# Kernel tuning notes

Hardware: AMD Instinct MI355X
Metric: run time of the kernel (lower is better)

The kernel has to match this reference:

```python
import jax, jax.numpy as jnp
import numpy as np

CAPACITY = 1024


def setup_inputs() -> dict:
    T, H, I, E, K = 2048, 1024, 1408, 8, 2
    key = jax.random.key(0)
    k0, k1, k2, k3, k4 = jax.random.split(key, 5)
    hidden_states = jax.random.normal(k0, (T, H), dtype=jnp.float32)
    w1 = jax.random.normal(k1, (E, 2 * I, H), dtype=jnp.float32) * 0.02  # [gate; up]
    w2 = jax.random.normal(k2, (E, H, I), dtype=jnp.float32) * 0.02
    topk_weights = jax.random.uniform(k3, (T, K), dtype=jnp.float32)
    topk_ids = jax.random.randint(k4, (T, K), 0, E, dtype=jnp.int32)
    return {"hidden_states": hidden_states, "w1": w1, "w2": w2,
            "topk_weights": topk_weights, "topk_ids": topk_ids}


def reference(hidden_states, w1, w2, topk_weights, topk_ids):
    # MoE: prepare(dispatch) -> grouped expert GEMM (silu-gated MLP) -> finalize(combine)
    T, H = hidden_states.shape
    E = w1.shape[0]
    I = w2.shape[2]
    K = topk_ids.shape[1]
    C = CAPACITY

    # ---- prepare: dispatch token copies to per-expert buffers ----
    flat_ids = topk_ids.reshape(-1)                       # (T*K,)
    onehot = jax.nn.one_hot(flat_ids, E, dtype=jnp.int32)  # (T*K, E)
    cs = jnp.cumsum(onehot, axis=0)                        # running per-expert counts
    pos = jnp.take_along_axis(cs, flat_ids[:, None], axis=1)[:, 0] - 1  # slot in expert buffer
    keep = pos < C
    pos_c = jnp.where(keep, pos, 0)

    x_flat = jnp.repeat(hidden_states, K, axis=0)          # (T*K, H)
    x_e = jnp.zeros((E, C, H), dtype=hidden_states.dtype)
    x_e = x_e.at[flat_ids, pos_c].add(jnp.where(keep[:, None], x_flat, 0.0))

    # ---- grouped expert GEMM: silu(gate) * up, then down-proj ----
    h = jnp.einsum('ech,eoh->eco', x_e, w1)                # (E, C, 2I)
    gate, up = h[..., :I], h[..., I:]
    act = jax.nn.silu(gate) * up                           # (E, C, I)
    y = jnp.einsum('eci,ehi->ech', act, w2)                # (E, C, H)

    # ---- finalize: gather back, apply router weights, reduce over top-k ----
    y_flat = y[flat_ids, pos_c] * (keep[:, None].astype(y.dtype)) \
             * topk_weights.reshape(-1, 1)                 # (T*K, H)
    out = y_flat.reshape(T, K, H).sum(axis=1)              # (T, H)
    return out.astype(hidden_states.dtype)
```

## Files before the change

kernel.cpp:

```cpp
#include <hip/hip_runtime.h>

#define NE 8
#define CAP 1024
#define HD 1024
#define ID 1408
#define TT 2048

typedef __attribute__((ext_vector_type(8))) short bf16x8;
typedef __attribute__((ext_vector_type(4))) float f32x4;
typedef unsigned short u16;
typedef unsigned int u32;
typedef unsigned long long u64;

__device__ __forceinline__ u16 f2bf(float f) {
  u32 u = __float_as_uint(f);
  u = (u + 0x7fffu + ((u >> 16) & 1u)) >> 16;
  return (u16)u;
}

__device__ __forceinline__ bf16x8 pack8(float4 a, float4 b) {
  bf16x8 r;
  r[0] = (short)f2bf(a.x); r[1] = (short)f2bf(a.y);
  r[2] = (short)f2bf(a.z); r[3] = (short)f2bf(a.w);
  r[4] = (short)f2bf(b.x); r[5] = (short)f2bf(b.y);
  r[6] = (short)f2bf(b.z); r[7] = (short)f2bf(b.w);
  return r;
}

__device__ __forceinline__ void async_cp16(const void* g, void* l) {
  __builtin_amdgcn_global_load_lds(
      (const __attribute__((address_space(1))) u32*)g,
      (__attribute__((address_space(3))) u32*)l, 16, 0, 0);
}

#define W1ROWS (NE * 2 * ID)
#define XBLK (TT * HD / 4 / 256)
__global__ __launch_bounds__(256) void prep_kernel(
    const float4* __restrict__ w1, ushort4* __restrict__ bw1,
    const float4* __restrict__ x, ushort4* __restrict__ bx,
    const int* __restrict__ ids, int* __restrict__ rowmap,
    int* __restrict__ counts) {
  int b = blockIdx.x;
  int tid = threadIdx.x;
  if (b == 0) {
    __shared__ unsigned char ids_s[TT * 2];
    __shared__ int sc[256][NE + 1];
    for (int i = tid; i < TT * 2; i += 256) ids_s[i] = (unsigned char)ids[i];
    __syncthreads();
    int base = tid * 16;
    u64 own64 = 0;
#pragma unroll
    for (int j = 0; j < 16; ++j) own64 += 1ull << (ids_s[base + j] * 8);
    int own[NE];
#pragma unroll
    for (int e = 0; e < NE; ++e) {
      own[e] = (int)((own64 >> (e * 8)) & 0xff);
      sc[tid][e] = own[e];
    }
    __syncthreads();
    for (int off = 1; off < 256; off <<= 1) {
      int v[NE];
      if (tid >= off) {
#pragma unroll
        for (int e = 0; e < NE; ++e) v[e] = sc[tid - off][e];
      }
      __syncthreads();
      if (tid >= off) {
#pragma unroll
        for (int e = 0; e < NE; ++e) sc[tid][e] += v[e];
      }
      __syncthreads();
    }
    if (tid == 255) {
#pragma unroll
      for (int e = 0; e < NE; ++e) counts[e] = sc[255][e] < CAP ? sc[255][e] : CAP;
    }
    int excl[NE];
#pragma unroll
    for (int e = 0; e < NE; ++e) excl[e] = sc[tid][e] - own[e];
    __syncthreads();
#pragma unroll
    for (int e = 0; e < NE; ++e) sc[tid][e] = excl[e];
#pragma unroll
    for (int j = 0; j < 16; ++j) {
      int f = base + j;
      int e = ids_s[f];
      int p = sc[tid][e]++;
      if (p < CAP) rowmap[e * CAP + p] = f;
    }
    return;
  }
  int bb = b - 1;
  if (bb < W1ROWS) {
    int n = bb % (2 * ID);
    int e = bb / (2 * ID);
    int j = (n < ID) ? n : (n - ID);
    int np = (j >> 4) * 32 + (j & 15) + ((n < ID) ? 0 : 16);
    float4 v = w1[((size_t)e * 2 * ID + n) * (HD / 4) + tid];
    ushort4 o;
    o.x = f2bf(v.x); o.y = f2bf(v.y); o.z = f2bf(v.z); o.w = f2bf(v.w);
    bw1[((size_t)e * 2 * ID + np) * (HD / 4) + tid] = o;
  } else {
    size_t i = (size_t)(bb - W1ROWS) * 256 + tid;
    float4 v = x[i];
    ushort4 o;
    o.x = f2bf(v.x); o.y = f2bf(v.y); o.z = f2bf(v.z); o.w = f2bf(v.w);
    bx[i] = o;
  }
}

#define G1BUF 24576
__global__ __launch_bounds__(256) void gemm1_kernel(
    const u16* __restrict__ A, const u16* __restrict__ B, u16* __restrict__ Hb,
    const int* __restrict__ rowmap, const int* __restrict__ counts,
    const float4* __restrict__ W2, bf16x8* __restrict__ bw2,
    float4* __restrict__ outz) {
  int bid = blockIdx.x;
  int tid = threadIdx.x;
  if (bid < 704) {
#pragma unroll
    for (int k2 = 0; k2 < 4; ++k2) {
      size_t base4 = ((size_t)bid * 4 + k2) * 1024;
      float4 v0 = W2[base4 + tid * 2];
      float4 v1 = W2[base4 + tid * 2 + 1];
      float4 v2 = W2[base4 + 512 + tid * 2];
      float4 v3 = W2[base4 + 512 + tid * 2 + 1];
      bf16x8* dst = bw2 + base4 / 2;
      dst[tid] = pack8(v0, v1);
      dst[256 + tid] = pack8(v2, v3);
    }
    return;
  }
  if (bid < 768) {
    size_t base = (size_t)(bid - 704) * 8192;
    float4 z = {0.f, 0.f, 0.f, 0.f};
#pragma unroll
    for (int i2 = 0; i2 < 32; ++i2) outz[base + i2 * 256 + tid] = z;
    return;
  }
  int g = bid - 768;
  int e = g & 7;
  int m0 = ((g >> 3) & 15) * 64;
  int n0 = (g >> 7) * 128;
  int count = counts[e];
  if (m0 >= count) return;
  int lane = tid & 63, wid = tid >> 6;
  int wm = wid >> 1, wn = wid & 1;
  int q = lane >> 4, lm = lane & 15;

  __shared__ __align__(16) char sm[3 * G1BUF];

  int rloc = tid >> 3;
  int chs = ((tid & 7) ^ (rloc & 7)) * 8;
  const u16* aP[2];
  const u16* bP[4];
#pragma unroll
  for (int i = 0; i < 2; ++i) {
    int gr = m0 + rloc + 32 * i;
    int f = (gr < count) ? rowmap[e * CAP + gr] : 0;
    aP[i] = A + (size_t)(f >> 1) * HD + chs;
  }
#pragma unroll
  for (int i = 0; i < 4; ++i)
    bP[i] = B + ((size_t)e * 2 * ID + n0 + rloc + 32 * i) * HD + chs;

  f32x4 zero = {0.f, 0.f, 0.f, 0.f};
  f32x4 acc[2][4];
#pragma unroll
  for (int mi = 0; mi < 2; ++mi)
#pragma unroll
    for (int ni = 0; ni < 4; ++ni) acc[mi][ni] = zero;

#define STAGE1(base, kt)                                             \
  do {                                                               \
    int ko_ = (kt) * 64;                                             \
    char* sb_ = (base);                                              \
    async_cp16(aP[0] + ko_, sb_ + (0 * 256 + tid) * 16);             \
    async_cp16(aP[1] + ko_, sb_ + (1 * 256 + tid) * 16);             \
    async_cp16(bP[0] + ko_, sb_ + 8192 + (0 * 256 + tid) * 16);      \
    async_cp16(bP[1] + ko_, sb_ + 8192 + (1 * 256 + tid) * 16);      \
    async_cp16(bP[2] + ko_, sb_ + 8192 + (2 * 256 + tid) * 16);      \
    async_cp16(bP[3] + ko_, sb_ + 8192 + (3 * 256 + tid) * 16);      \
  } while (0)

  STAGE1(sm, 0);
  STAGE1(sm + G1BUF, 1);
  int p = 0, pn2 = 2;
  for (int kt = 0; kt < HD / 64; ++kt) {
    if (kt == HD / 64 - 1)
      asm volatile("s_waitcnt vmcnt(0)\ns_barrier" ::: "memory");
    else
      asm volatile("s_waitcnt vmcnt(6)\ns_barrier" ::: "memory");
    const char* sb = sm + p * G1BUF;
    if (kt + 2 < HD / 64) STAGE1(sm + pn2 * G1BUF, kt + 2);
#pragma unroll
    for (int s = 0; s < 2; ++s) {
      int cs = ((s * 4 + q) ^ (lm & 7)) * 16;
      bf16x8 af[2], bfr[4];
#pragma unroll
      for (int mi = 0; mi < 2; ++mi)
        af[mi] = *(const bf16x8*)(sb + (wm * 32 + mi * 16 + lm) * 128 + cs);
#pragma unroll
      for (int ni = 0; ni < 4; ++ni)
        bfr[ni] = *(const bf16x8*)(sb + 8192 + (wn * 64 + ni * 16 + lm) * 128 + cs);
      __builtin_amdgcn_s_setprio(1);
#pragma unroll
      for (int mi = 0; mi < 2; ++mi)
#pragma unroll
        for (int ni = 0; ni < 4; ++ni)
          acc[mi][ni] = __builtin_amdgcn_mfma_f32_16x16x32_bf16(af[mi], bfr[ni], acc[mi][ni], 0, 0, 0);
      __builtin_amdgcn_s_setprio(0);
    }
    p = (p == 2) ? 0 : p + 1;
    pn2 = (pn2 == 2) ? 0 : pn2 + 1;
  }
  __syncthreads();

  u16* smOut = (u16*)sm;
#pragma unroll
  for (int mi = 0; mi < 2; ++mi) {
#pragma unroll
    for (int k = 0; k < 2; ++k) {
      int colL = wn * 32 + k * 16 + lm;
#pragma unroll
      for (int r = 0; r < 4; ++r) {
        float g2 = acc[mi][2 * k][r];
        float u = acc[mi][2 * k + 1][r];
        float a = g2 / (1.f + __expf(-g2)) * u;
        int row = wm * 32 + mi * 16 + q * 4 + r;
        smOut[row * 72 + colL] = f2bf(a);
      }
    }
  }
  __syncthreads();
  {
    int row = tid >> 2, seg = tid & 3;
    const u16* sp = smOut + row * 72 + seg * 16;
    bf16x8 v0 = *(const bf16x8*)sp;
    bf16x8 v1 = *(const bf16x8*)(sp + 8);
    u16* dp = Hb + ((size_t)e * CAP + m0 + row) * ID + (n0 >> 1) + seg * 16;
    *(bf16x8*)dp = v0;
    *(bf16x8*)(dp + 8) = v1;
  }
}

#define G2BUF 16384
__global__ __launch_bounds__(256) void gemm2_kernel(
    const u16* __restrict__ A, const u16* __restrict__ B, float* __restrict__ out,
    const int* __restrict__ rowmap, const int* __restrict__ counts,
    const float* __restrict__ tw) {
  int e = blockIdx.x;
  int count = counts[e];
  int m0 = blockIdx.y * 64;
  if (m0 >= count) return;
  int n0 = blockIdx.z * 64;
  int tid = threadIdx.x;
  int lane = tid & 63, wid = tid >> 6;
  int wm = wid >> 1, wn = wid & 1;
  int q = lane >> 4, lm = lane & 15;

  __shared__ __align__(16) char sm[3 * G2BUF];

  int rloc = tid >> 3;
  int chs = ((tid & 7) ^ (rloc & 7)) * 8;
  const u16* aP[2];
  const u16* bP[2];
#pragma unroll
  for (int i = 0; i < 2; ++i) {
    aP[i] = A + ((size_t)e * CAP + m0 + rloc + 32 * i) * ID + chs;
    bP[i] = B + ((size_t)e * HD + n0 + rloc + 32 * i) * ID + chs;
  }

  f32x4 zero = {0.f, 0.f, 0.f, 0.f};
  f32x4 acc[2][2];
#pragma unroll
  for (int mi = 0; mi < 2; ++mi)
#pragma unroll
    for (int ni = 0; ni < 2; ++ni) acc[mi][ni] = zero;

#define STAGE2(base, kt)                                             \
  do {                                                               \
    int ko_ = (kt) * 64;                                             \
    char* sb_ = (base);                                              \
    async_cp16(aP[0] + ko_, sb_ + (0 * 256 + tid) * 16);             \
    async_cp16(aP[1] + ko_, sb_ + (1 * 256 + tid) * 16);             \
    async_cp16(bP[0] + ko_, sb_ + 8192 + (0 * 256 + tid) * 16);      \
    async_cp16(bP[1] + ko_, sb_ + 8192 + (1 * 256 + tid) * 16);      \
  } while (0)

  STAGE2(sm, 0);
  STAGE2(sm + G2BUF, 1);
  int p = 0, pn2 = 2;
  for (int kt = 0; kt < ID / 64; ++kt) {
    if (kt == ID / 64 - 1)
      asm volatile("s_waitcnt vmcnt(0)\ns_barrier" ::: "memory");
    else
      asm volatile("s_waitcnt vmcnt(4)\ns_barrier" ::: "memory");
    const char* sb = sm + p * G2BUF;
    if (kt + 2 < ID / 64) STAGE2(sm + pn2 * G2BUF, kt + 2);
#pragma unroll
    for (int s = 0; s < 2; ++s) {
      int cs = ((s * 4 + q) ^ (lm & 7)) * 16;
      bf16x8 af[2], bfr[2];
#pragma unroll
      for (int mi = 0; mi < 2; ++mi)
        af[mi] = *(const bf16x8*)(sb + (wm * 32 + mi * 16 + lm) * 128 + cs);
#pragma unroll
      for (int ni = 0; ni < 2; ++ni)
        bfr[ni] = *(const bf16x8*)(sb + 8192 + (wn * 32 + ni * 16 + lm) * 128 + cs);
      __builtin_amdgcn_s_setprio(1);
#pragma unroll
      for (int mi = 0; mi < 2; ++mi)
#pragma unroll
        for (int ni = 0; ni < 2; ++ni)
          acc[mi][ni] = __builtin_amdgcn_mfma_f32_16x16x32_bf16(af[mi], bfr[ni], acc[mi][ni], 0, 0, 0);
      __builtin_amdgcn_s_setprio(0);
    }
    p = (p == 2) ? 0 : p + 1;
    pn2 = (pn2 == 2) ? 0 : pn2 + 1;
  }

#pragma unroll
  for (int mi = 0; mi < 2; ++mi) {
#pragma unroll
    for (int r = 0; r < 4; ++r) {
      int grow = m0 + wm * 32 + mi * 16 + q * 4 + r;
      if (grow < count) {
        int f = rowmap[e * CAP + grow];
        float w = tw[f];
        int t = f >> 1;
#pragma unroll
        for (int ni = 0; ni < 2; ++ni) {
          int col = n0 + wn * 32 + ni * 16 + lm;
          atomicAdd(&out[(size_t)t * HD + col], w * acc[mi][ni][r]);
        }
      }
    }
  }
}

extern "C" void kernel_launch(void* const* d_in, const int* in_sizes, int n_in,
                              void* d_out, int out_size, void* d_ws, size_t ws_size,
                              hipStream_t stream) {
  const float* hidden = (const float*)d_in[0];
  const float* w1 = (const float*)d_in[1];
  const float* w2 = (const float*)d_in[2];
  const float* tw = (const float*)d_in[3];
  const int* ids = (const int*)d_in[4];
  float* out = (float*)d_out;

  char* p = (char*)d_ws;
  auto alloc = [&](size_t b) { char* r = p; p += (b + 255) & ~(size_t)255; return r; };
  u16* bw1 = (u16*)alloc((size_t)NE * 2 * ID * HD * 2);
  u16* bw2 = (u16*)alloc((size_t)NE * HD * ID * 2);
  u16* bx = (u16*)alloc((size_t)TT * HD * 2);
  u16* hbuf = (u16*)alloc((size_t)NE * CAP * ID * 2);
  int* rowmap = (int*)alloc((size_t)NE * CAP * 4);
  int* counts = (int*)alloc((size_t)NE * 4);

  prep_kernel<<<1 + W1ROWS + XBLK, 256, 0, stream>>>(
      (const float4*)w1, (ushort4*)bw1, (const float4*)hidden, (ushort4*)bx,
      ids, rowmap, counts);

  gemm1_kernel<<<768 + NE * (CAP / 64) * (2 * ID / 128), 256, 0, stream>>>(
      bx, bw1, hbuf, rowmap, counts, (const float4*)w2, (bf16x8*)bw2,
      (float4*)out);

  gemm2_kernel<<<dim3(NE, CAP / 64, HD / 64), 256, 0, stream>>>(
      hbuf, bw2, out, rowmap, counts, tw);
}
```

Before: 256.7 us.

## Merge three MoE kernels into one persistent cooperative kernel with grid syncs

Replaces the prep, gate/up GEMM and down GEMM launches with a single persistent kernel. It runs the three phases in a grid-stride loop over tiles and separates them with cooperative grid syncs. The grid is capped at 512 blocks based on occupancy. If the cooperative launch fails, it falls back to three phased launches. This is meant to remove launch gaps and tail idle time between stages, at the cost of fewer resident blocks, grid-barrier overhead and a persistent loop that may balance GEMM tiles less well than one block per tile.

```diff
diff --git a/kernel.cpp b/kernel.cpp
--- a/kernel.cpp
+++ b/kernel.cpp
@@ -1,4 +1,5 @@
 #include <hip/hip_runtime.h>
+#include <hip/hip_cooperative_groups.h>
 
 #define NE 8
 #define CAP 1024
@@ -33,143 +34,14 @@
       (__attribute__((address_space(3))) u32*)l, 16, 0, 0);
 }
 
-#define W1ROWS (NE * 2 * ID)
-#define XBLK (TT * HD / 4 / 256)
-__global__ __launch_bounds__(256) void prep_kernel(
-    const float4* __restrict__ w1, ushort4* __restrict__ bw1,
-    const float4* __restrict__ x, ushort4* __restrict__ bx,
-    const int* __restrict__ ids, int* __restrict__ rowmap,
-    int* __restrict__ counts) {
-  int b = blockIdx.x;
-  int tid = threadIdx.x;
-  if (b == 0) {
-    __shared__ unsigned char ids_s[TT * 2];
-    __shared__ int sc[256][NE + 1];
-    for (int i = tid; i < TT * 2; i += 256) ids_s[i] = (unsigned char)ids[i];
-    __syncthreads();
-    int base = tid * 16;
-    u64 own64 = 0;
-#pragma unroll
-    for (int j = 0; j < 16; ++j) own64 += 1ull << (ids_s[base + j] * 8);
-    int own[NE];
-#pragma unroll
-    for (int e = 0; e < NE; ++e) {
-      own[e] = (int)((own64 >> (e * 8)) & 0xff);
-      sc[tid][e] = own[e];
-    }
-    __syncthreads();
-    for (int off = 1; off < 256; off <<= 1) {
-      int v[NE];
-      if (tid >= off) {
-#pragma unroll
-        for (int e = 0; e < NE; ++e) v[e] = sc[tid - off][e];
-      }
-      __syncthreads();
-      if (tid >= off) {
-#pragma unroll
-        for (int e = 0; e < NE; ++e) sc[tid][e] += v[e];
-      }
-      __syncthreads();
-    }
-    if (tid == 255) {
-#pragma unroll
-      for (int e = 0; e < NE; ++e) counts[e] = sc[255][e] < CAP ? sc[255][e] : CAP;
-    }
-    int excl[NE];
-#pragma unroll
-    for (int e = 0; e < NE; ++e) excl[e] = sc[tid][e] - own[e];
-    __syncthreads();
-#pragma unroll
-    for (int e = 0; e < NE; ++e) sc[tid][e] = excl[e];
-#pragma unroll
-    for (int j = 0; j < 16; ++j) {
-      int f = base + j;
-      int e = ids_s[f];
-      int p = sc[tid][e]++;
-      if (p < CAP) rowmap[e * CAP + p] = f;
-    }
-    return;
-  }
-  int bb = b - 1;
-  if (bb < W1ROWS) {
-    int n = bb % (2 * ID);
-    int e = bb / (2 * ID);
-    int j = (n < ID) ? n : (n - ID);
-    int np = (j >> 4) * 32 + (j & 15) + ((n < ID) ? 0 : 16);
-    float4 v = w1[((size_t)e * 2 * ID + n) * (HD / 4) + tid];
-    ushort4 o;
-    o.x = f2bf(v.x); o.y = f2bf(v.y); o.z = f2bf(v.z); o.w = f2bf(v.w);
-    bw1[((size_t)e * 2 * ID + np) * (HD / 4) + tid] = o;
-  } else {
-    size_t i = (size_t)(bb - W1ROWS) * 256 + tid;
-    float4 v = x[i];
-    ushort4 o;
-    o.x = f2bf(v.x); o.y = f2bf(v.y); o.z = f2bf(v.z); o.w = f2bf(v.w);
-    bx[i] = o;
-  }
-}
-
+#define W1U (NE * 2 * ID)
+#define XU (TT * HD / 1024)
+#define PTOT (W1U + XU)
+#define G1TILES (NE * (CAP / 64) * (2 * ID / 128))
+#define G1TOT (768 + G1TILES)
+#define G2TILES (NE * (CAP / 64) * (HD / 64))
 #define G1BUF 24576
-__global__ __launch_bounds__(256) void gemm1_kernel(
-    const u16* __restrict__ A, const u16* __restrict__ B, u16* __restrict__ Hb,
-    const int* __restrict__ rowmap, const int* __restrict__ counts,
-    const float4* __restrict__ W2, bf16x8* __restrict__ bw2,
-    float4* __restrict__ outz) {
-  int bid = blockIdx.x;
-  int tid = threadIdx.x;
-  if (bid < 704) {
-#pragma unroll
-    for (int k2 = 0; k2 < 4; ++k2) {
-      size_t base4 = ((size_t)bid * 4 + k2) * 1024;
-      float4 v0 = W2[base4 + tid * 2];
-      float4 v1 = W2[base4 + tid * 2 + 1];
-      float4 v2 = W2[base4 + 512 + tid * 2];
-      float4 v3 = W2[base4 + 512 + tid * 2 + 1];
-      bf16x8* dst = bw2 + base4 / 2;
-      dst[tid] = pack8(v0, v1);
-      dst[256 + tid] = pack8(v2, v3);
-    }
-    return;
-  }
-  if (bid < 768) {
-    size_t base = (size_t)(bid - 704) * 8192;
-    float4 z = {0.f, 0.f, 0.f, 0.f};
-#pragma unroll
-    for (int i2 = 0; i2 < 32; ++i2) outz[base + i2 * 256 + tid] = z;
-    return;
-  }
-  int g = bid - 768;
-  int e = g & 7;
-  int m0 = ((g >> 3) & 15) * 64;
-  int n0 = (g >> 7) * 128;
-  int count = counts[e];
-  if (m0 >= count) return;
-  int lane = tid & 63, wid = tid >> 6;
-  int wm = wid >> 1, wn = wid & 1;
-  int q = lane >> 4, lm = lane & 15;
-
-  __shared__ __align__(16) char sm[3 * G1BUF];
-
-  int rloc = tid >> 3;
-  int chs = ((tid & 7) ^ (rloc & 7)) * 8;
-  const u16* aP[2];
-  const u16* bP[4];
-#pragma unroll
-  for (int i = 0; i < 2; ++i) {
-    int gr = m0 + rloc + 32 * i;
-    int f = (gr < count) ? rowmap[e * CAP + gr] : 0;
-    aP[i] = A + (size_t)(f >> 1) * HD + chs;
-  }
-#pragma unroll
-  for (int i = 0; i < 4; ++i)
-    bP[i] = B + ((size_t)e * 2 * ID + n0 + rloc + 32 * i) * HD + chs;
-
-  f32x4 zero = {0.f, 0.f, 0.f, 0.f};
-  f32x4 acc[2][4];
-#pragma unroll
-  for (int mi = 0; mi < 2; ++mi)
-#pragma unroll
-    for (int ni = 0; ni < 4; ++ni) acc[mi][ni] = zero;
+#define G2BUF 16384
 
 #define STAGE1(base, kt)                                             \
   do {                                                               \
@@ -183,101 +55,6 @@
     async_cp16(bP[3] + ko_, sb_ + 8192 + (3 * 256 + tid) * 16);      \
   } while (0)
 
-  STAGE1(sm, 0);
-  STAGE1(sm + G1BUF, 1);
-  int p = 0, pn2 = 2;
-  for (int kt = 0; kt < HD / 64; ++kt) {
-    if (kt == HD / 64 - 1)
-      asm volatile("s_waitcnt vmcnt(0)\ns_barrier" ::: "memory");
-    else
-      asm volatile("s_waitcnt vmcnt(6)\ns_barrier" ::: "memory");
-    const char* sb = sm + p * G1BUF;
-    if (kt + 2 < HD / 64) STAGE1(sm + pn2 * G1BUF, kt + 2);
-#pragma unroll
-    for (int s = 0; s < 2; ++s) {
-      int cs = ((s * 4 + q) ^ (lm & 7)) * 16;
-      bf16x8 af[2], bfr[4];
-#pragma unroll
-      for (int mi = 0; mi < 2; ++mi)
-        af[mi] = *(const bf16x8*)(sb + (wm * 32 + mi * 16 + lm) * 128 + cs);
-#pragma unroll
-      for (int ni = 0; ni < 4; ++ni)
-        bfr[ni] = *(const bf16x8*)(sb + 8192 + (wn * 64 + ni * 16 + lm) * 128 + cs);
-      __builtin_amdgcn_s_setprio(1);
-#pragma unroll
-      for (int mi = 0; mi < 2; ++mi)
-#pragma unroll
-        for (int ni = 0; ni < 4; ++ni)
-          acc[mi][ni] = __builtin_amdgcn_mfma_f32_16x16x32_bf16(af[mi], bfr[ni], acc[mi][ni], 0, 0, 0);
-      __builtin_amdgcn_s_setprio(0);
-    }
-    p = (p == 2) ? 0 : p + 1;
-    pn2 = (pn2 == 2) ? 0 : pn2 + 1;
-  }
-  __syncthreads();
-
-  u16* smOut = (u16*)sm;
-#pragma unroll
-  for (int mi = 0; mi < 2; ++mi) {
-#pragma unroll
-    for (int k = 0; k < 2; ++k) {
-      int colL = wn * 32 + k * 16 + lm;
-#pragma unroll
-      for (int r = 0; r < 4; ++r) {
-        float g2 = acc[mi][2 * k][r];
-        float u = acc[mi][2 * k + 1][r];
-        float a = g2 / (1.f + __expf(-g2)) * u;
-        int row = wm * 32 + mi * 16 + q * 4 + r;
-        smOut[row * 72 + colL] = f2bf(a);
-      }
-    }
-  }
-  __syncthreads();
-  {
-    int row = tid >> 2, seg = tid & 3;
-    const u16* sp = smOut + row * 72 + seg * 16;
-    bf16x8 v0 = *(const bf16x8*)sp;
-    bf16x8 v1 = *(const bf16x8*)(sp + 8);
-    u16* dp = Hb + ((size_t)e * CAP + m0 + row) * ID + (n0 >> 1) + seg * 16;
-    *(bf16x8*)dp = v0;
-    *(bf16x8*)(dp + 8) = v1;
-  }
-}
-
-#define G2BUF 16384
-__global__ __launch_bounds__(256) void gemm2_kernel(
-    const u16* __restrict__ A, const u16* __restrict__ B, float* __restrict__ out,
-    const int* __restrict__ rowmap, const int* __restrict__ counts,
-    const float* __restrict__ tw) {
-  int e = blockIdx.x;
-  int count = counts[e];
-  int m0 = blockIdx.y * 64;
-  if (m0 >= count) return;
-  int n0 = blockIdx.z * 64;
-  int tid = threadIdx.x;
-  int lane = tid & 63, wid = tid >> 6;
-  int wm = wid >> 1, wn = wid & 1;
-  int q = lane >> 4, lm = lane & 15;
-
-  __shared__ __align__(16) char sm[3 * G2BUF];
-
-  int rloc = tid >> 3;
-  int chs = ((tid & 7) ^ (rloc & 7)) * 8;
-  const u16* aP[2];
-  const u16* bP[2];
-#pragma unroll
-  for (int i = 0; i < 2; ++i) {
-    aP[i] = A + ((size_t)e * CAP + m0 + rloc + 32 * i) * ID + chs;
-    bP[i] = B + ((size_t)e * HD + n0 + rloc + 32 * i) * ID + chs;
-  }
-
-  f32x4 zero = {0.f, 0.f, 0.f, 0.f};
-  f32x4 acc[2][2];
-#pragma unroll
-  for (int mi = 0; mi < 2; ++mi)
-#pragma unroll
-    for (int ni = 0; ni < 2; ++ni) acc[mi][ni] = zero;
-
 #define STAGE2(base, kt)                                             \
   do {                                                               \
     int ko_ = (kt) * 64;                                             \
@@ -288,53 +65,311 @@
     async_cp16(bP[1] + ko_, sb_ + 8192 + (1 * 256 + tid) * 16);      \
   } while (0)
 
-  STAGE2(sm, 0);
-  STAGE2(sm + G2BUF, 1);
-  int p = 0, pn2 = 2;
-  for (int kt = 0; kt < ID / 64; ++kt) {
-    if (kt == ID / 64 - 1)
-      asm volatile("s_waitcnt vmcnt(0)\ns_barrier" ::: "memory");
-    else
-      asm volatile("s_waitcnt vmcnt(4)\ns_barrier" ::: "memory");
-    const char* sb = sm + p * G2BUF;
-    if (kt + 2 < ID / 64) STAGE2(sm + pn2 * G2BUF, kt + 2);
-#pragma unroll
-    for (int s = 0; s < 2; ++s) {
-      int cs = ((s * 4 + q) ^ (lm & 7)) * 16;
-      bf16x8 af[2], bfr[2];
+__global__ __launch_bounds__(256, 2) void mega_kernel(
+    const float4* __restrict__ x32, const float4* __restrict__ w1,
+    const float4* __restrict__ w2, const float* __restrict__ tw,
+    const int* __restrict__ ids, float* __restrict__ out,
+    ushort4* __restrict__ bw1, bf16x8* __restrict__ bw2,
+    ushort4* __restrict__ bx, u16* __restrict__ hbuf,
+    int* __restrict__ rowmap, int* __restrict__ counts, int phase) {
+  __shared__ __align__(16) char sm[3 * G1BUF];
+  int bid = blockIdx.x, nb = gridDim.x, tid = threadIdx.x;
+
+  if (phase == -1 || phase == 0) {
+    if (bid == 0) {
+      unsigned char* ids_s = (unsigned char*)sm;
+      int(*sc)[NE + 1] = (int(*)[NE + 1])(sm + 4096);
+      for (int i = tid; i < TT * 2; i += 256) ids_s[i] = (unsigned char)ids[i];
+      __syncthreads();
+      int base = tid * 16;
+      u64 own64 = 0;
+#pragma unroll
+      for (int j = 0; j < 16; ++j) own64 += 1ull << (ids_s[base + j] * 8);
+      int own[NE];
+#pragma unroll
+      for (int e = 0; e < NE; ++e) {
+        own[e] = (int)((own64 >> (e * 8)) & 0xff);
+        sc[tid][e] = own[e];
+      }
+      __syncthreads();
+      for (int off = 1; off < 256; off <<= 1) {
+        int v[NE];
+        if (tid >= off) {
+#pragma unroll
+          for (int e = 0; e < NE; ++e) v[e] = sc[tid - off][e];
+        }
+        __syncthreads();
+        if (tid >= off) {
+#pragma unroll
+          for (int e = 0; e < NE; ++e) sc[tid][e] += v[e];
+        }
+        __syncthreads();
+      }
+      if (tid == 255) {
+#pragma unroll
+        for (int e = 0; e < NE; ++e) counts[e] = sc[255][e] < CAP ? sc[255][e] : CAP;
+      }
+      int excl[NE];
+#pragma unroll
+      for (int e = 0; e < NE; ++e) excl[e] = sc[tid][e] - own[e];
+      __syncthreads();
+#pragma unroll
+      for (int e = 0; e < NE; ++e) sc[tid][e] = excl[e];
+#pragma unroll
+      for (int j = 0; j < 16; ++j) {
+        int f = base + j;
+        int e = ids_s[f];
+        int p = sc[tid][e]++;
+        if (p < CAP) rowmap[e * CAP + p] = f;
+      }
+      __syncthreads();
+    } else {
+      int stride = nb - 1;
+      for (int u0 = bid - 1; u0 < PTOT; u0 += 4 * stride) {
+        float4 v[4];
+        ushort4* dp[4];
+        bool ok[4];
+#pragma unroll
+        for (int k = 0; k < 4; ++k) {
+          int u = u0 + k * stride;
+          ok[k] = (u < PTOT);
+          if (ok[k]) {
+            const float4* sp;
+            ushort4* dd;
+            if (u < W1U) {
+              int e = u / (2 * ID);
+              int n = u - e * (2 * ID);
+              int jj = (n < ID) ? n : (n - ID);
+              int np = (jj >> 4) * 32 + (jj & 15) + ((n < ID) ? 0 : 16);
+              sp = w1 + ((size_t)e * (2 * ID) + n) * (HD / 4);
+              dd = bw1 + ((size_t)e * (2 * ID) + np) * (HD / 4);
+            } else {
+              int xi = u - W1U;
+              sp = x32 + (size_t)xi * 256;
+              dd = bx + (size_t)xi * 256;
+            }
+            v[k] = sp[tid];
+            dp[k] = dd + tid;
+          }
+        }
+#pragma unroll
+        for (int k = 0; k < 4; ++k)
+          if (ok[k]) {
+            ushort4 o;
+            o.x = f2bf(v[k].x); o.y = f2bf(v[k].y);
+            o.z = f2bf(v[k].z); o.w = f2bf(v[k].w);
+            *dp[k] = o;
+          }
+      }
+    }
+  }
+  if (phase == -1) {
+    __threadfence();
+    cooperative_groups::this_grid().sync();
+  }
+
+  if (phase == -1 || phase == 1) {
+    for (int idx = bid; idx < G1TOT; idx += nb) {
+      if (idx < 704) {
+#pragma unroll
+        for (int k2 = 0; k2 < 4; ++k2) {
+          size_t base4 = ((size_t)idx * 4 + k2) * 1024;
+          float4 v0 = w2[base4 + tid * 2];
+          float4 v1 = w2[base4 + tid * 2 + 1];
+          float4 v2 = w2[base4 + 512 + tid * 2];
+          float4 v3 = w2[base4 + 512 + tid * 2 + 1];
+          bf16x8* dst = bw2 + base4 / 2;
+          dst[tid] = pack8(v0, v1);
+          dst[256 + tid] = pack8(v2, v3);
+        }
+        continue;
+      }
+      if (idx < 768) {
+        size_t base = (size_t)(idx - 704) * 8192;
+        float4 z = {0.f, 0.f, 0.f, 0.f};
+        float4* o4 = (float4*)out;
+#pragma unroll
+        for (int i2 = 0; i2 < 32; ++i2) o4[base + i2 * 256 + tid] = z;
+        continue;
+      }
+      int g = idx - 768;
+      int e = g & 7;
+      int m0 = ((g >> 3) & 15) * 64;
+      int n0 = (g >> 7) * 128;
+      int count = counts[e];
+      if (m0 >= count) continue;
+      int lane = tid & 63, wid = tid >> 6;
+      int wm = wid >> 1, wn = wid & 1;
+      int q = lane >> 4, lm = lane & 15;
+      int rloc = tid >> 3;
+      int chs = ((tid & 7) ^ (rloc & 7)) * 8;
+      const u16* A = (const u16*)bx;
+      const u16* B = (const u16*)bw1;
+      const u16* aP[2];
+      const u16* bP[4];
+#pragma unroll
+      for (int i = 0; i < 2; ++i) {
+        int gr = m0 + rloc + 32 * i;
+        int f = (gr < count) ? rowmap[e * CAP + gr] : 0;
+        aP[i] = A + (size_t)(f >> 1) * HD + chs;
+      }
+#pragma unroll
+      for (int i = 0; i < 4; ++i)
+        bP[i] = B + ((size_t)e * 2 * ID + n0 + rloc + 32 * i) * HD + chs;
+
+      f32x4 zero = {0.f, 0.f, 0.f, 0.f};
+      f32x4 acc[2][4];
 #pragma unroll
       for (int mi = 0; mi < 2; ++mi)
-        af[mi] = *(const bf16x8*)(sb + (wm * 32 + mi * 16 + lm) * 128 + cs);
-#pragma unroll
-      for (int ni = 0; ni < 2; ++ni)
-        bfr[ni] = *(const bf16x8*)(sb + 8192 + (wn * 32 + ni * 16 + lm) * 128 + cs);
-      __builtin_amdgcn_s_setprio(1);
+#pragma unroll
+        for (int ni = 0; ni < 4; ++ni) acc[mi][ni] = zero;
+
+      STAGE1(sm, 0);
+      STAGE1(sm + G1BUF, 1);
+      int p = 0, pn2 = 2;
+      for (int kt = 0; kt < HD / 64; ++kt) {
+        if (kt == HD / 64 - 1)
+          asm volatile("s_waitcnt vmcnt(0)\ns_barrier" ::: "memory");
+        else
+          asm volatile("s_waitcnt vmcnt(6)\ns_barrier" ::: "memory");
+        const char* sb = sm + p * G1BUF;
+        if (kt + 2 < HD / 64) STAGE1(sm + pn2 * G1BUF, kt + 2);
+#pragma unroll
+        for (int s = 0; s < 2; ++s) {
+          int cs = ((s * 4 + q) ^ (lm & 7)) * 16;
+          bf16x8 af[2], bfr[4];
+#pragma unroll
+          for (int mi = 0; mi < 2; ++mi)
+            af[mi] = *(const bf16x8*)(sb + (wm * 32 + mi * 16 + lm) * 128 + cs);
+#pragma unroll
+          for (int ni = 0; ni < 4; ++ni)
+            bfr[ni] = *(const bf16x8*)(sb + 8192 + (wn * 64 + ni * 16 + lm) * 128 + cs);
+          __builtin_amdgcn_s_setprio(1);
+#pragma unroll
+          for (int mi = 0; mi < 2; ++mi)
+#pragma unroll
+            for (int ni = 0; ni < 4; ++ni)
+              acc[mi][ni] = __builtin_amdgcn_mfma_f32_16x16x32_bf16(af[mi], bfr[ni], acc[mi][ni], 0, 0, 0);
+          __builtin_amdgcn_s_setprio(0);
+        }
+        p = (p == 2) ? 0 : p + 1;
+        pn2 = (pn2 == 2) ? 0 : pn2 + 1;
+      }
+      __syncthreads();
+
+      u16* smOut = (u16*)sm;
+#pragma unroll
+      for (int mi = 0; mi < 2; ++mi) {
+#pragma unroll
+        for (int k = 0; k < 2; ++k) {
+          int colL = wn * 32 + k * 16 + lm;
+#pragma unroll
+          for (int r = 0; r < 4; ++r) {
+            float g2 = acc[mi][2 * k][r];
+            float u = acc[mi][2 * k + 1][r];
+            float a = g2 / (1.f + __expf(-g2)) * u;
+            int row = wm * 32 + mi * 16 + q * 4 + r;
+            smOut[row * 72 + colL] = f2bf(a);
+          }
+        }
+      }
+      __syncthreads();
+      {
+        int row = tid >> 2, seg = tid & 3;
+        const u16* sp = smOut + row * 72 + seg * 16;
+        bf16x8 v0 = *(const bf16x8*)sp;
+        bf16x8 v1 = *(const bf16x8*)(sp + 8);
+        u16* dp = hbuf + ((size_t)e * CAP + m0 + row) * ID + (n0 >> 1) + seg * 16;
+        *(bf16x8*)dp = v0;
+        *(bf16x8*)(dp + 8) = v1;
+      }
+      __syncthreads();
+    }
+  }
+  if (phase == -1) {
+    __threadfence();
+    cooperative_groups::this_grid().sync();
+  }
+
+  if (phase == -1 || phase == 2) {
+    for (int idx = bid; idx < G2TILES; idx += nb) {
+      int e = idx & 7;
+      int m0 = ((idx >> 3) & 15) * 64;
+      int n0 = (idx >> 7) * 64;
+      int count = counts[e];
+      if (m0 >= count) continue;
+      int lane = tid & 63, wid = tid >> 6;
+      int wm = wid >> 1, wn = wid & 1;
+      int q = lane >> 4, lm = lane & 15;
+      int rloc = tid >> 3;
+      int chs = ((tid & 7) ^ (rloc & 7)) * 8;
+      const u16* A = hbuf;
+      const u16* B = (const u16*)bw2;
+      const u16* aP[2];
+      const u16* bP[2];
+#pragma unroll
+      for (int i = 0; i < 2; ++i) {
+        aP[i] = A + ((size_t)e * CAP + m0 + rloc + 32 * i) * ID + chs;
+        bP[i] = B + ((size_t)e * HD + n0 + rloc + 32 * i) * ID + chs;
+      }
+
+      f32x4 zero = {0.f, 0.f, 0.f, 0.f};
+      f32x4 acc[2][2];
 #pragma unroll
       for (int mi = 0; mi < 2; ++mi)
 #pragma unroll
-        for (int ni = 0; ni < 2; ++ni)
-          acc[mi][ni] = __builtin_amdgcn_mfma_f32_16x16x32_bf16(af[mi], bfr[ni], acc[mi][ni], 0, 0, 0);
-      __builtin_amdgcn_s_setprio(0);
-    }
-    p = (p == 2) ? 0 : p + 1;
-    pn2 = (pn2 == 2) ? 0 : pn2 + 1;
-  }
-
-#pragma unroll
-  for (int mi = 0; mi < 2; ++mi) {
-#pragma unroll
-    for (int r = 0; r < 4; ++r) {
-      int grow = m0 + wm * 32 + mi * 16 + q * 4 + r;
-      if (grow < count) {
-        int f = rowmap[e * CAP + grow];
-        float w = tw[f];
-        int t = f >> 1;
-#pragma unroll
-        for (int ni = 0; ni < 2; ++ni) {
-          int col = n0 + wn * 32 + ni * 16 + lm;
-          atomicAdd(&out[(size_t)t * HD + col], w * acc[mi][ni][r]);
-        }
-      }
+        for (int ni = 0; ni < 2; ++ni) acc[mi][ni] = zero;
+
+      STAGE2(sm, 0);
+      STAGE2(sm + G2BUF, 1);
+      int p = 0, pn2 = 2;
+      for (int kt = 0; kt < ID / 64; ++kt) {
+        if (kt == ID / 64 - 1)
+          asm volatile("s_waitcnt vmcnt(0)\ns_barrier" ::: "memory");
+        else
+          asm volatile("s_waitcnt vmcnt(4)\ns_barrier" ::: "memory");
+        const char* sb = sm + p * G2BUF;
+        if (kt + 2 < ID / 64) STAGE2(sm + pn2 * G2BUF, kt + 2);
+#pragma unroll
+        for (int s = 0; s < 2; ++s) {
+          int cs = ((s * 4 + q) ^ (lm & 7)) * 16;
+          bf16x8 af[2], bfr[2];
+#pragma unroll
+          for (int mi = 0; mi < 2; ++mi)
+            af[mi] = *(const bf16x8*)(sb + (wm * 32 + mi * 16 + lm) * 128 + cs);
+#pragma unroll
+          for (int ni = 0; ni < 2; ++ni)
+            bfr[ni] = *(const bf16x8*)(sb + 8192 + (wn * 32 + ni * 16 + lm) * 128 + cs);
+          __builtin_amdgcn_s_setprio(1);
+#pragma unroll
+          for (int mi = 0; mi < 2; ++mi)
+#pragma unroll
+            for (int ni = 0; ni < 2; ++ni)
+              acc[mi][ni] = __builtin_amdgcn_mfma_f32_16x16x32_bf16(af[mi], bfr[ni], acc[mi][ni], 0, 0, 0);
+          __builtin_amdgcn_s_setprio(0);
+        }
+        p = (p == 2) ? 0 : p + 1;
+        pn2 = (pn2 == 2) ? 0 : pn2 + 1;
+      }
+
+#pragma unroll
+      for (int mi = 0; mi < 2; ++mi) {
+#pragma unroll
+        for (int r = 0; r < 4; ++r) {
+          int grow = m0 + wm * 32 + mi * 16 + q * 4 + r;
+          if (grow < count) {
+            int f = rowmap[e * CAP + grow];
+            float w = tw[f];
+            int t = f >> 1;
+#pragma unroll
+            for (int ni = 0; ni < 2; ++ni) {
+              int col = n0 + wn * 32 + ni * 16 + lm;
+              atomicAdd(&out[(size_t)t * HD + col], w * acc[mi][ni][r]);
+            }
+          }
+        }
+      }
+      __syncthreads();
     }
   }
 }
@@ -342,30 +377,42 @@
 extern "C" void kernel_launch(void* const* d_in, const int* in_sizes, int n_in,
                               void* d_out, int out_size, void* d_ws, size_t ws_size,
                               hipStream_t stream) {
-  const float* hidden = (const float*)d_in[0];
-  const float* w1 = (const float*)d_in[1];
-  const float* w2 = (const float*)d_in[2];
+  const float4* x32 = (const float4*)d_in[0];
+  const float4* w1 = (const float4*)d_in[1];
+  const float4* w2 = (const float4*)d_in[2];
   const float* tw = (const float*)d_in[3];
   const int* ids = (const int*)d_in[4];
   float* out = (float*)d_out;
 
   char* p = (char*)d_ws;
   auto alloc = [&](size_t b) { char* r = p; p += (b + 255) & ~(size_t)255; return r; };
-  u16* bw1 = (u16*)alloc((size_t)NE * 2 * ID * HD * 2);
-  u16* bw2 = (u16*)alloc((size_t)NE * HD * ID * 2);
-  u16* bx = (u16*)alloc((size_t)TT * HD * 2);
+  ushort4* bw1 = (ushort4*)alloc((size_t)NE * 2 * ID * HD * 2);
+  bf16x8* bw2 = (bf16x8*)alloc((size_t)NE * HD * ID * 2);
+  ushort4* bx = (ushort4*)alloc((size_t)TT * HD * 2);
   u16* hbuf = (u16*)alloc((size_t)NE * CAP * ID * 2);
   int* rowmap = (int*)alloc((size_t)NE * CAP * 4);
   int* counts = (int*)alloc((size_t)NE * 4);
 
-  prep_kernel<<<1 + W1ROWS + XBLK, 256, 0, stream>>>(
-      (const float4*)w1, (ushort4*)bw1, (const float4*)hidden, (ushort4*)bx,
-      ids, rowmap, counts);
-
-  gemm1_kernel<<<768 + NE * (CAP / 64) * (2 * ID / 128), 256, 0, stream>>>(
-      bx, bw1, hbuf, rowmap, counts, (const float4*)w2, (bf16x8*)bw2,
-      (float4*)out);
-
-  gemm2_kernel<<<dim3(NE, CAP / 64, HD / 64), 256, 0, stream>>>(
-      hbuf, bw2, out, rowmap, counts, tw);
+  static int gblk = 0;
+  if (gblk == 0) {
+    int nbmax = 0;
+    hipOccupancyMaxActiveBlocksPerMultiprocessor(&nbmax, mega_kernel, 256, 0);
+    if (nbmax < 1) nbmax = 1;
+    gblk = nbmax * 256;
+    if (gblk > 512) gblk = 512;
+  }
+
+  int ph = -1;
+  void* args[] = {&x32, &w1, &w2, &tw, &ids, &out, &bw1, &bw2,
+                  &bx,  &hbuf, &rowmap, &counts, &ph};
+  hipError_t err = hipLaunchCooperativeKernel(
+      mega_kernel, dim3(gblk), dim3(256), args, 0, stream);
+  if (err != hipSuccess) {
+    mega_kernel<<<512, 256, 0, stream>>>(x32, w1, w2, tw, ids, out, bw1, bw2,
+                                         bx, hbuf, rowmap, counts, 0);
+    mega_kernel<<<512, 256, 0, stream>>>(x32, w1, w2, tw, ids, out, bw1, bw2,
+                                         bx, hbuf, rowmap, counts, 1);
+    mega_kernel<<<512, 256, 0, stream>>>(x32, w1, w2, tw, ids, out, bw1, bw2,
+                                         bx, hbuf, rowmap, counts, 2);
+  }
 }
```

Result: slower. 555.3 us (+116.3%).

## Use persistent M-loop grids for expert GEMMs and interleave W2 conversion blocks

Applied to the files above, without the earlier changes.

Both expert GEMMs now launch a fixed grid of 10 M-slots per expert and column tile, and each block loops over M tiles with a stride of 640 rows. This replaces the earlier grid that launched all 16 M tiles and relied on early exit when a tile was past the expert's count. In gemm1 the W2 bf16 conversion blocks are interleaved with the GEMM blocks in a 2-of-7 pattern instead of running all first, so conversion traffic overlaps compute. Zeroing of the output moves into the prep kernel. The aim is fewer idle launched blocks and better balance, with the risk of per-block serial tails for experts that hold more than 640 rows.

```diff
diff --git a/kernel.cpp b/kernel.cpp
--- a/kernel.cpp
+++ b/kernel.cpp
@@ -35,11 +35,12 @@
 
 #define W1ROWS (NE * 2 * ID)
 #define XBLK (TT * HD / 4 / 256)
+#define OZB (TT * HD / 4 / 256)
 __global__ __launch_bounds__(256) void prep_kernel(
     const float4* __restrict__ w1, ushort4* __restrict__ bw1,
     const float4* __restrict__ x, ushort4* __restrict__ bx,
     const int* __restrict__ ids, int* __restrict__ rowmap,
-    int* __restrict__ counts) {
+    int* __restrict__ counts, float4* __restrict__ outz) {
   int b = blockIdx.x;
   int tid = threadIdx.x;
   if (b == 0) {
@@ -100,12 +101,16 @@
     ushort4 o;
     o.x = f2bf(v.x); o.y = f2bf(v.y); o.z = f2bf(v.z); o.w = f2bf(v.w);
     bw1[((size_t)e * 2 * ID + np) * (HD / 4) + tid] = o;
-  } else {
+  } else if (bb < W1ROWS + XBLK) {
     size_t i = (size_t)(bb - W1ROWS) * 256 + tid;
     float4 v = x[i];
     ushort4 o;
     o.x = f2bf(v.x); o.y = f2bf(v.y); o.z = f2bf(v.z); o.w = f2bf(v.w);
     bx[i] = o;
+  } else {
+    size_t i = (size_t)(bb - W1ROWS - XBLK) * 256 + tid;
+    float4 z = {0.f, 0.f, 0.f, 0.f};
+    outz[i] = z;
   }
 }
 
@@ -113,14 +118,16 @@
 __global__ __launch_bounds__(256) void gemm1_kernel(
     const u16* __restrict__ A, const u16* __restrict__ B, u16* __restrict__ Hb,
     const int* __restrict__ rowmap, const int* __restrict__ counts,
-    const float4* __restrict__ W2, bf16x8* __restrict__ bw2,
-    float4* __restrict__ outz) {
+    const float4* __restrict__ W2, bf16x8* __restrict__ bw2) {
   int bid = blockIdx.x;
   int tid = threadIdx.x;
-  if (bid < 704) {
+  int grp = bid >> 3, sub = bid & 7;
+  int q7 = grp / 7, r7 = grp - q7 * 7;
+  if (r7 == 2 || r7 == 5) {
+    int r = (q7 * 2 + (r7 == 5 ? 1 : 0)) * 8 + sub;
 #pragma unroll
     for (int k2 = 0; k2 < 4; ++k2) {
-      size_t base4 = ((size_t)bid * 4 + k2) * 1024;
+      size_t base4 = ((size_t)r * 4 + k2) * 1024;
       float4 v0 = W2[base4 + tid * 2];
       float4 v1 = W2[base4 + tid * 2 + 1];
       float4 v2 = W2[base4 + 512 + tid * 2];
@@ -131,19 +138,11 @@
     }
     return;
   }
-  if (bid < 768) {
-    size_t base = (size_t)(bid - 704) * 8192;
-    float4 z = {0.f, 0.f, 0.f, 0.f};
-#pragma unroll
-    for (int i2 = 0; i2 < 32; ++i2) outz[base + i2 * 256 + tid] = z;
-    return;
-  }
-  int g = bid - 768;
-  int e = g & 7;
-  int m0 = ((g >> 3) & 15) * 64;
-  int n0 = (g >> 7) * 128;
+  int tg = q7 * 5 + r7 - (r7 > 2 ? 1 : 0) - (r7 > 5 ? 1 : 0);
+  int e = sub;
+  int my = tg % 10;
+  int n0 = (tg / 10) * 128;
   int count = counts[e];
-  if (m0 >= count) return;
   int lane = tid & 63, wid = tid >> 6;
   int wm = wid >> 1, wn = wid & 1;
   int q = lane >> 4, lm = lane & 15;
@@ -152,24 +151,10 @@
 
   int rloc = tid >> 3;
   int chs = ((tid & 7) ^ (rloc & 7)) * 8;
-  const u16* aP[2];
   const u16* bP[4];
-#pragma unroll
-  for (int i = 0; i < 2; ++i) {
-    int gr = m0 + rloc + 32 * i;
-    int f = (gr < count) ? rowmap[e * CAP + gr] : 0;
-    aP[i] = A + (size_t)(f >> 1) * HD + chs;
-  }
 #pragma unroll
   for (int i = 0; i < 4; ++i)
     bP[i] = B + ((size_t)e * 2 * ID + n0 + rloc + 32 * i) * HD + chs;
-
-  f32x4 zero = {0.f, 0.f, 0.f, 0.f};
-  f32x4 acc[2][4];
-#pragma unroll
-  for (int mi = 0; mi < 2; ++mi)
-#pragma unroll
-    for (int ni = 0; ni < 4; ++ni) acc[mi][ni] = zero;
 
 #define STAGE1(base, kt)                                             \
   do {                                                               \
@@ -183,64 +168,82 @@
     async_cp16(bP[3] + ko_, sb_ + 8192 + (3 * 256 + tid) * 16);      \
   } while (0)
 
-  STAGE1(sm, 0);
-  STAGE1(sm + G1BUF, 1);
-  int p = 0, pn2 = 2;
-  for (int kt = 0; kt < HD / 64; ++kt) {
-    if (kt == HD / 64 - 1)
-      asm volatile("s_waitcnt vmcnt(0)\ns_barrier" ::: "memory");
-    else
-      asm volatile("s_waitcnt vmcnt(6)\ns_barrier" ::: "memory");
-    const char* sb = sm + p * G1BUF;
-    if (kt + 2 < HD / 64) STAGE1(sm + pn2 * G1BUF, kt + 2);
-#pragma unroll
-    for (int s = 0; s < 2; ++s) {
-      int cs = ((s * 4 + q) ^ (lm & 7)) * 16;
-      bf16x8 af[2], bfr[4];
-#pragma unroll
-      for (int mi = 0; mi < 2; ++mi)
-        af[mi] = *(const bf16x8*)(sb + (wm * 32 + mi * 16 + lm) * 128 + cs);
-#pragma unroll
-      for (int ni = 0; ni < 4; ++ni)
-        bfr[ni] = *(const bf16x8*)(sb + 8192 + (wn * 64 + ni * 16 + lm) * 128 + cs);
-      __builtin_amdgcn_s_setprio(1);
-#pragma unroll
-      for (int mi = 0; mi < 2; ++mi)
+  for (int m0 = my * 64; m0 < count; m0 += 640) {
+    const u16* aP[2];
+#pragma unroll
+    for (int i = 0; i < 2; ++i) {
+      int gr = m0 + rloc + 32 * i;
+      int f = (gr < count) ? rowmap[e * CAP + gr] : 0;
+      aP[i] = A + (size_t)(f >> 1) * HD + chs;
+    }
+
+    f32x4 zero = {0.f, 0.f, 0.f, 0.f};
+    f32x4 acc[2][4];
+#pragma unroll
+    for (int mi = 0; mi < 2; ++mi)
+#pragma unroll
+      for (int ni = 0; ni < 4; ++ni) acc[mi][ni] = zero;
+
+    STAGE1(sm, 0);
+    STAGE1(sm + G1BUF, 1);
+    int p = 0, pn2 = 2;
+    for (int kt = 0; kt < HD / 64; ++kt) {
+      if (kt == HD / 64 - 1)
+        asm volatile("s_waitcnt vmcnt(0)\ns_barrier" ::: "memory");
+      else
+        asm volatile("s_waitcnt vmcnt(6)\ns_barrier" ::: "memory");
+      const char* sb = sm + p * G1BUF;
+      if (kt + 2 < HD / 64) STAGE1(sm + pn2 * G1BUF, kt + 2);
+#pragma unroll
+      for (int s = 0; s < 2; ++s) {
+        int cs = ((s * 4 + q) ^ (lm & 7)) * 16;
+        bf16x8 af[2], bfr[4];
+#pragma unroll
+        for (int mi = 0; mi < 2; ++mi)
+          af[mi] = *(const bf16x8*)(sb + (wm * 32 + mi * 16 + lm) * 128 + cs);
 #pragma unroll
         for (int ni = 0; ni < 4; ++ni)
-          acc[mi][ni] = __builtin_amdgcn_mfma_f32_16x16x32_bf16(af[mi], bfr[ni], acc[mi][ni], 0, 0, 0);
-      __builtin_amdgcn_s_setprio(0);
-    }
-    p = (p == 2) ? 0 : p + 1;
-    pn2 = (pn2 == 2) ? 0 : pn2 + 1;
-  }
-  __syncthreads();
-
-  u16* smOut = (u16*)sm;
-#pragma unroll
-  for (int mi = 0; mi < 2; ++mi) {
-#pragma unroll
-    for (int k = 0; k < 2; ++k) {
-      int colL = wn * 32 + k * 16 + lm;
-#pragma unroll
-      for (int r = 0; r < 4; ++r) {
-        float g2 = acc[mi][2 * k][r];
-        float u = acc[mi][2 * k + 1][r];
-        float a = g2 / (1.f + __expf(-g2)) * u;
-        int row = wm * 32 + mi * 16 + q * 4 + r;
-        smOut[row * 72 + colL] = f2bf(a);
-      }
-    }
-  }
-  __syncthreads();
-  {
-    int row = tid >> 2, seg = tid & 3;
-    const u16* sp = smOut + row * 72 + seg * 16;
-    bf16x8 v0 = *(const bf16x8*)sp;
-    bf16x8 v1 = *(const bf16x8*)(sp + 8);
-    u16* dp = Hb + ((size_t)e * CAP + m0 + row) * ID + (n0 >> 1) + seg * 16;
-    *(bf16x8*)dp = v0;
-    *(bf16x8*)(dp + 8) = v1;
+          bfr[ni] = *(const bf16x8*)(sb + 8192 + (wn * 64 + ni * 16 + lm) * 128 + cs);
+        __builtin_amdgcn_s_setprio(1);
+#pragma unroll
+        for (int mi = 0; mi < 2; ++mi)
+#pragma unroll
+          for (int ni = 0; ni < 4; ++ni)
+            acc[mi][ni] = __builtin_amdgcn_mfma_f32_16x16x32_bf16(af[mi], bfr[ni], acc[mi][ni], 0, 0, 0);
+        __builtin_amdgcn_s_setprio(0);
+      }
+      p = (p == 2) ? 0 : p + 1;
+      pn2 = (pn2 == 2) ? 0 : pn2 + 1;
+    }
+    __syncthreads();
+
+    u16* smOut = (u16*)sm;
+#pragma unroll
+    for (int mi = 0; mi < 2; ++mi) {
+#pragma unroll
+      for (int k = 0; k < 2; ++k) {
+        int colL = wn * 32 + k * 16 + lm;
+#pragma unroll
+        for (int r = 0; r < 4; ++r) {
+          float g2 = acc[mi][2 * k][r];
+          float u = acc[mi][2 * k + 1][r];
+          float a = g2 / (1.f + __expf(-g2)) * u;
+          int row = wm * 32 + mi * 16 + q * 4 + r;
+          smOut[row * 72 + colL] = f2bf(a);
+        }
+      }
+    }
+    __syncthreads();
+    {
+      int row = tid >> 2, seg = tid & 3;
+      const u16* sp = smOut + row * 72 + seg * 16;
+      bf16x8 v0 = *(const bf16x8*)sp;
+      bf16x8 v1 = *(const bf16x8*)(sp + 8);
+      u16* dp = Hb + ((size_t)e * CAP + m0 + row) * ID + (n0 >> 1) + seg * 16;
+      *(bf16x8*)dp = v0;
+      *(bf16x8*)(dp + 8) = v1;
+    }
+    __syncthreads();
   }
 }
 
@@ -249,11 +252,12 @@
     const u16* __restrict__ A, const u16* __restrict__ B, float* __restrict__ out,
     const int* __restrict__ rowmap, const int* __restrict__ counts,
     const float* __restrict__ tw) {
-  int e = blockIdx.x;
+  int idx = blockIdx.x;
+  int e = idx & 7;
+  int tg = idx >> 3;
+  int my = tg % 10;
+  int n0 = (tg / 10) * 64;
   int count = counts[e];
-  int m0 = blockIdx.y * 64;
-  if (m0 >= count) return;
-  int n0 = blockIdx.z * 64;
   int tid = threadIdx.x;
   int lane = tid & 63, wid = tid >> 6;
   int wm = wid >> 1, wn = wid & 1;
@@ -263,20 +267,10 @@
 
   int rloc = tid >> 3;
   int chs = ((tid & 7) ^ (rloc & 7)) * 8;
-  const u16* aP[2];
   const u16* bP[2];
 #pragma unroll
-  for (int i = 0; i < 2; ++i) {
-    aP[i] = A + ((size_t)e * CAP + m0 + rloc + 32 * i) * ID + chs;
+  for (int i = 0; i < 2; ++i)
     bP[i] = B + ((size_t)e * HD + n0 + rloc + 32 * i) * ID + chs;
-  }
-
-  f32x4 zero = {0.f, 0.f, 0.f, 0.f};
-  f32x4 acc[2][2];
-#pragma unroll
-  for (int mi = 0; mi < 2; ++mi)
-#pragma unroll
-    for (int ni = 0; ni < 2; ++ni) acc[mi][ni] = zero;
 
 #define STAGE2(base, kt)                                             \
   do {                                                               \
@@ -288,54 +282,69 @@
     async_cp16(bP[1] + ko_, sb_ + 8192 + (1 * 256 + tid) * 16);      \
   } while (0)
 
-  STAGE2(sm, 0);
-  STAGE2(sm + G2BUF, 1);
-  int p = 0, pn2 = 2;
-  for (int kt = 0; kt < ID / 64; ++kt) {
-    if (kt == ID / 64 - 1)
-      asm volatile("s_waitcnt vmcnt(0)\ns_barrier" ::: "memory");
-    else
-      asm volatile("s_waitcnt vmcnt(4)\ns_barrier" ::: "memory");
-    const char* sb = sm + p * G2BUF;
-    if (kt + 2 < ID / 64) STAGE2(sm + pn2 * G2BUF, kt + 2);
-#pragma unroll
-    for (int s = 0; s < 2; ++s) {
-      int cs = ((s * 4 + q) ^ (lm & 7)) * 16;
-      bf16x8 af[2], bfr[2];
-#pragma unroll
-      for (int mi = 0; mi < 2; ++mi)
-        af[mi] = *(const bf16x8*)(sb + (wm * 32 + mi * 16 + lm) * 128 + cs);
-#pragma unroll
-      for (int ni = 0; ni < 2; ++ni)
-        bfr[ni] = *(const bf16x8*)(sb + 8192 + (wn * 32 + ni * 16 + lm) * 128 + cs);
-      __builtin_amdgcn_s_setprio(1);
-#pragma unroll
-      for (int mi = 0; mi < 2; ++mi)
+  for (int m0 = my * 64; m0 < count; m0 += 640) {
+    const u16* aP[2];
+#pragma unroll
+    for (int i = 0; i < 2; ++i)
+      aP[i] = A + ((size_t)e * CAP + m0 + rloc + 32 * i) * ID + chs;
+
+    f32x4 zero = {0.f, 0.f, 0.f, 0.f};
+    f32x4 acc[2][2];
+#pragma unroll
+    for (int mi = 0; mi < 2; ++mi)
+#pragma unroll
+      for (int ni = 0; ni < 2; ++ni) acc[mi][ni] = zero;
+
+    STAGE2(sm, 0);
+    STAGE2(sm + G2BUF, 1);
+    int p = 0, pn2 = 2;
+    for (int kt = 0; kt < ID / 64; ++kt) {
+      if (kt == ID / 64 - 1)
+        asm volatile("s_waitcnt vmcnt(0)\ns_barrier" ::: "memory");
+      else
+        asm volatile("s_waitcnt vmcnt(4)\ns_barrier" ::: "memory");
+      const char* sb = sm + p * G2BUF;
+      if (kt + 2 < ID / 64) STAGE2(sm + pn2 * G2BUF, kt + 2);
+#pragma unroll
+      for (int s = 0; s < 2; ++s) {
+        int cs = ((s * 4 + q) ^ (lm & 7)) * 16;
+        bf16x8 af[2], bfr[2];
+#pragma unroll
+        for (int mi = 0; mi < 2; ++mi)
+          af[mi] = *(const bf16x8*)(sb + (wm * 32 + mi * 16 + lm) * 128 + cs);
 #pragma unroll
         for (int ni = 0; ni < 2; ++ni)
-          acc[mi][ni] = __builtin_amdgcn_mfma_f32_16x16x32_bf16(af[mi], bfr[ni], acc[mi][ni], 0, 0, 0);
-      __builtin_amdgcn_s_setprio(0);
-    }
-    p = (p == 2) ? 0 : p + 1;
-    pn2 = (pn2 == 2) ? 0 : pn2 + 1;
-  }
-
-#pragma unroll
-  for (int mi = 0; mi < 2; ++mi) {
-#pragma unroll
-    for (int r = 0; r < 4; ++r) {
-      int grow = m0 + wm * 32 + mi * 16 + q * 4 + r;
-      if (grow < count) {
-        int f = rowmap[e * CAP + grow];
-        float w = tw[f];
-        int t = f >> 1;
-#pragma unroll
-        for (int ni = 0; ni < 2; ++ni) {
-          int col = n0 + wn * 32 + ni * 16 + lm;
-          atomicAdd(&out[(size_t)t * HD + col], w * acc[mi][ni][r]);
+          bfr[ni] = *(const bf16x8*)(sb + 8192 + (wn * 32 + ni * 16 + lm) * 128 + cs);
+        __builtin_amdgcn_s_setprio(1);
+#pragma unroll
+        for (int mi = 0; mi < 2; ++mi)
+#pragma unroll
+          for (int ni = 0; ni < 2; ++ni)
+            acc[mi][ni] = __builtin_amdgcn_mfma_f32_16x16x32_bf16(af[mi], bfr[ni], acc[mi][ni], 0, 0, 0);
+        __builtin_amdgcn_s_setprio(0);
+      }
+      p = (p == 2) ? 0 : p + 1;
+      pn2 = (pn2 == 2) ? 0 : pn2 + 1;
+    }
+
+#pragma unroll
+    for (int mi = 0; mi < 2; ++mi) {
+#pragma unroll
+      for (int r = 0; r < 4; ++r) {
+        int grow = m0 + wm * 32 + mi * 16 + q * 4 + r;
+        if (grow < count) {
+          int f = rowmap[e * CAP + grow];
+          float w = tw[f];
+          int t = f >> 1;
+#pragma unroll
+          for (int ni = 0; ni < 2; ++ni) {
+            int col = n0 + wn * 32 + ni * 16 + lm;
+            atomicAdd(&out[(size_t)t * HD + col], w * acc[mi][ni][r]);
+          }
         }
       }
     }
+    __syncthreads();
   }
 }
 
@@ -358,14 +367,13 @@
   int* rowmap = (int*)alloc((size_t)NE * CAP * 4);
   int* counts = (int*)alloc((size_t)NE * 4);
 
-  prep_kernel<<<1 + W1ROWS + XBLK, 256, 0, stream>>>(
+  prep_kernel<<<1 + W1ROWS + XBLK + OZB, 256, 0, stream>>>(
       (const float4*)w1, (ushort4*)bw1, (const float4*)hidden, (ushort4*)bx,
-      ids, rowmap, counts);
-
-  gemm1_kernel<<<768 + NE * (CAP / 64) * (2 * ID / 128), 256, 0, stream>>>(
-      bx, bw1, hbuf, rowmap, counts, (const float4*)w2, (bf16x8*)bw2,
-      (float4*)out);
-
-  gemm2_kernel<<<dim3(NE, CAP / 64, HD / 64), 256, 0, stream>>>(
+      ids, rowmap, counts, (float4*)out);
+
+  gemm1_kernel<<<308 * 8, 256, 0, stream>>>(
+      bx, bw1, hbuf, rowmap, counts, (const float4*)w2, (bf16x8*)bw2);
+
+  gemm2_kernel<<<8 * 10 * 16, 256, 0, stream>>>(
       hbuf, bw2, out, rowmap, counts, tw);
 }
```

Measured after the change: 250.6 us. 1.02x faster.
